# Kernel tuning notes

Hardware: AMD Instinct MI355X
Metric: run time of the kernel (lower is better)

The kernel has to match this reference:

```python
import jax, jax.numpy as jnp
import numpy as np
import math

NUM_HEADS = 8
LN_EPS = 1e-5
SINK_EPS = 1.0  # entropic eps in SinkhornDistance (eps=1)


def _layer_norm(x, g, b):
    m = jnp.mean(x, axis=-1, keepdims=True)
    v = jnp.var(x, axis=-1, keepdims=True)
    return (x - m) * jax.lax.rsqrt(v + LN_EPS) * g + b


def setup_inputs() -> dict:
    key = jax.random.key(0)
    ks = jax.random.split(key, 8)
    B, n, dQ, dV = 8, 1024, 512, 512
    s = 1.0 / math.sqrt(dV)
    return {
        "Q": jax.random.normal(ks[0], (B, n, dQ), jnp.float32),
        "K": jax.random.normal(ks[1], (B, n, dQ), jnp.float32),
        "Wq": jax.random.normal(ks[2], (dV, dQ), jnp.float32) * s,
        "bq": jax.random.normal(ks[3], (dV,), jnp.float32) * 0.01,
        "Wo": jax.random.normal(ks[4], (dV, dV), jnp.float32) * s,
        "bo": jax.random.normal(ks[5], (dV,), jnp.float32) * 0.01,
        "g0": jnp.ones((dV,), jnp.float32),
        "b0": jnp.zeros((dV,), jnp.float32),
        "g1": jnp.ones((dV,), jnp.float32),
        "b1": jnp.zeros((dV,), jnp.float32),
    }


def reference(Q, K, Wq, bq, Wo, bo, g0, b0, g1, b1):
    # K is accepted by the original forward but unused (K_ = V_ = Q_).
    B, n, _ = Q.shape
    dim_V = Wq.shape[0]
    H = NUM_HEADS
    d = dim_V // H

    Qp = Q @ Wq.T + bq                                   # [B, n, dim_V]
    # torch.cat(Q.split(d, 2), 0): head-major stacking -> [H*B, n, d]
    Q_ = Qp.reshape(B, n, H, d).transpose(2, 0, 1, 3).reshape(H * B, n, d)

    sqrtV = math.sqrt(math.sqrt(dim_V))
    X = Q_ / sqrtV
    # cost = dotmat(X, X) = -X X^T  (overall scaled by 1/sqrt(dim_V))
    C = -jnp.einsum('bnd,bmd->bnm', X, X)                # [HB, n, n]

    # log-domain Sinkhorn, eps=1, max_iter=1, mu = nu = 1/n
    log_mu = jnp.log(1.0 / n + 1e-8).astype(Q.dtype)
    M0 = -C / SINK_EPS
    u = SINK_EPS * (log_mu - jax.scipy.special.logsumexp(M0, axis=-1))         # [HB, n]
    v = SINK_EPS * (log_mu - jax.scipy.special.logsumexp(
        (-C + u[:, :, None]) / SINK_EPS, axis=1))                               # [HB, n]
    pi = jnp.exp((-C + u[:, :, None] + v[:, None, :]) / SINK_EPS)               # [HB, n, n]

    A = pi * n
    O_ = Q_ + jnp.einsum('bnm,bmd->bnd', A, Q_)          # [HB, n, d]
    # inverse head stacking -> [B, n, dim_V]
    O = O_.reshape(H, B, n, d).transpose(1, 2, 0, 3).reshape(B, n, dim_V)

    O = _layer_norm(O, g0, b0)
    O = O + jax.nn.relu(O @ Wo.T + bo)
    O = _layer_norm(O, g1, b1)
    return O
```

## Files before the change

kernel.cpp:

```cpp
#include <hip/hip_runtime.h>
#include <hip/hip_bf16.h>

typedef __bf16 bf16;
typedef __bf16 bf16x4 __attribute__((ext_vector_type(4)));
typedef __bf16 bf16x8 __attribute__((ext_vector_type(8)));
typedef float  f32x4  __attribute__((ext_vector_type(4)));
typedef float  f32x16 __attribute__((ext_vector_type(16)));
typedef unsigned int uint32x2 __attribute__((ext_vector_type(2)));

#define DEVI static __device__ __forceinline__

constexpr float SCALE2  = 0.063758716f;
constexpr float L2MU    = -9.9999852f;
constexpr int   LDT     = 72;

DEVI f32x4 mfma16(bf16x8 a, bf16x8 b, f32x4 c) {
    return __builtin_amdgcn_mfma_f32_16x16x32_bf16(a, b, c, 0, 0, 0);
}
DEVI f32x16 mfma32(bf16x8 a, bf16x8 b, f32x16 c) {
    return __builtin_amdgcn_mfma_f32_32x32x16_bf16(a, b, c, 0, 0, 0);
}
DEVI unsigned cvtpk(float lo, float hi) {
    unsigned r;
    asm("v_cvt_pk_bf16_f32 %0, %1, %2" : "=v"(r) : "v"(lo), "v"(hi));
    return r;
}

DEVI bf16x8 cvt8(const float* __restrict__ p) {
    const float4 f0 = *(const float4*)p;
    const float4 f1 = *(const float4*)(p + 4);
    bf16x8 h;
    h[0] = (bf16)f0.x; h[1] = (bf16)f0.y; h[2] = (bf16)f0.z; h[3] = (bf16)f0.w;
    h[4] = (bf16)f1.x; h[5] = (bf16)f1.y; h[6] = (bf16)f1.z; h[7] = (bf16)f1.w;
    return h;
}

__global__ __launch_bounds__(256)
void cvtw_kernel(const float* __restrict__ W, bf16* __restrict__ Wb)
{
    const int i = (blockIdx.x * 256 + threadIdx.x) * 8;
    *(bf16x8*)(&Wb[i]) = cvt8(W + i);
}

template<int EPI>
__global__ __launch_bounds__(256)
void gemm_kernel(const void* __restrict__ Ap, const bf16* __restrict__ Bb,
                 const float* __restrict__ bias, const bf16* __restrict__ X0,
                 bf16* __restrict__ outQh, bf16* __restrict__ outQhT,
                 float* __restrict__ outT)
{
    __shared__ bf16 sA[2][64 * LDT];
    __shared__ bf16 sB[2][64 * LDT];
    const int tid = threadIdx.x;
    const int lin = blockIdx.y * 8 + blockIdx.x;
    const int wk  = ((lin & 7) << 7) | (lin >> 3);
    const int rowBase = (wk >> 3) * 64;
    const int colBase = (wk & 7) * 64;
    const int w = tid >> 6, lane = tid & 63, quad = lane >> 4, l16 = lane & 15;
    const int wr = (w >> 1) * 32, wc = (w & 1) * 32;
    const int r0 = tid >> 3, kb0 = tid & 7;

    f32x4 acc[2][2];
    #pragma unroll
    for (int i = 0; i < 2; ++i)
        #pragma unroll
        for (int j = 0; j < 2; ++j)
            #pragma unroll
            for (int e = 0; e < 4; ++e) acc[i][j][e] = 0.f;

    #pragma unroll
    for (int it = 0; it < 2; ++it) {
        const int r = it * 32 + r0;
        if (EPI == 0)
            *(bf16x8*)(&sA[0][r * LDT + kb0 * 8]) =
                cvt8((const float*)Ap + (size_t)(rowBase + r) * 512 + kb0 * 8);
        else
            *(uint4*)(&sA[0][r * LDT + kb0 * 8]) =
                *(const uint4*)((const bf16*)Ap + (size_t)(rowBase + r) * 512 + kb0 * 8);
        *(uint4*)(&sB[0][r * LDT + kb0 * 8]) =
            *(const uint4*)(Bb + (size_t)(colBase + r) * 512 + kb0 * 8);
    }
    __syncthreads();

    for (int kt8 = 0; kt8 < 8; ++kt8) {
        const int cur = kt8 & 1;
        float4 pfa[2][2];
        uint4  pfa16[2], pfb[2];
        if (kt8 < 7) {
            const int kn = (kt8 + 1) * 64;
            #pragma unroll
            for (int it = 0; it < 2; ++it) {
                const int r = it * 32 + r0;
                if (EPI == 0) {
                    const float* ap = (const float*)Ap + (size_t)(rowBase + r) * 512 + kn + kb0 * 8;
                    pfa[it][0] = *(const float4*)ap;
                    pfa[it][1] = *(const float4*)(ap + 4);
                } else {
                    pfa16[it] = *(const uint4*)((const bf16*)Ap + (size_t)(rowBase + r) * 512 + kn + kb0 * 8);
                }
                pfb[it] = *(const uint4*)(Bb + (size_t)(colBase + r) * 512 + kn + kb0 * 8);
            }
        }

        #pragma unroll
        for (int kk = 0; kk < 2; ++kk) {
            bf16x8 a[2], b[2];
            #pragma unroll
            for (int i = 0; i < 2; ++i)
                a[i] = *(const bf16x8*)(&sA[cur][(wr + i * 16 + l16) * LDT + kk * 32 + quad * 8]);
            #pragma unroll
            for (int j = 0; j < 2; ++j)
                b[j] = *(const bf16x8*)(&sB[cur][(wc + j * 16 + l16) * LDT + kk * 32 + quad * 8]);
            #pragma unroll
            for (int i = 0; i < 2; ++i)
                #pragma unroll
                for (int j = 0; j < 2; ++j)
                    acc[i][j] = mfma16(a[i], b[j], acc[i][j]);
        }

        if (kt8 < 7) {
            #pragma unroll
            for (int it = 0; it < 2; ++it) {
                const int r = it * 32 + r0;
                if (EPI == 0) {
                    bf16x8 h;
                    h[0] = (bf16)pfa[it][0].x; h[1] = (bf16)pfa[it][0].y;
                    h[2] = (bf16)pfa[it][0].z; h[3] = (bf16)pfa[it][0].w;
                    h[4] = (bf16)pfa[it][1].x; h[5] = (bf16)pfa[it][1].y;
                    h[6] = (bf16)pfa[it][1].z; h[7] = (bf16)pfa[it][1].w;
                    *(bf16x8*)(&sA[cur ^ 1][r * LDT + kb0 * 8]) = h;
                } else {
                    *(uint4*)(&sA[cur ^ 1][r * LDT + kb0 * 8]) = pfa16[it];
                }
                *(uint4*)(&sB[cur ^ 1][r * LDT + kb0 * 8]) = pfb[it];
            }
        }
        __syncthreads();
    }

    #pragma unroll
    for (int i = 0; i < 2; ++i) {
        #pragma unroll
        for (int j = 0; j < 2; ++j) {
            const int col = colBase + wc + j * 16 + l16;
            const float bv = bias[col];
            if (EPI == 0) {
                const int hh = col >> 6, jj = col & 63;
                const int rowA = rowBase + wr + i * 16 + quad * 4;
                const int bb = rowA >> 10, iib = rowA & 1023;
                const int bhh = (hh << 3) + bb;
                bf16x4 pk;
                #pragma unroll
                for (int rg = 0; rg < 4; ++rg) {
                    const float z = acc[i][j][rg] + bv;
                    pk[rg] = (bf16)z;
                    outQh[((size_t)(bhh * 1024 + iib + rg) << 6) + jj] = (bf16)z;
                }
                if (outQhT)
                    *(bf16x4*)(&outQhT[(((size_t)bhh * 64 + jj) << 10) + iib]) = pk;
            } else {
                #pragma unroll
                for (int rg = 0; rg < 4; ++rg) {
                    const int row = rowBase + wr + i * 16 + quad * 4 + rg;
                    const float z = acc[i][j][rg] + bv;
                    const float x0 = (float)X0[(size_t)row * 512 + col];
                    outT[(size_t)row * 512 + col] = x0 + fmaxf(z, 0.f);
                }
            }
        }
    }
}

template<int ADD_U>
__global__ __launch_bounds__(256, 4)
void sink_lse_kernel(const bf16* __restrict__ Qh, const float* __restrict__ uin,
                     float* __restrict__ out)
{
    __shared__ bf16 sQm[2][64 * LDT];
    __shared__ float su[1024];
    const int tid = threadIdx.x;
    const int lin = blockIdx.y * 16 + blockIdx.x;
    const int wk  = ((lin & 7) << 7) | (lin >> 3);
    const int bh = wk >> 4;
    const int rowTile = (wk & 15) * 64;
    const bf16* Qb = Qh + ((size_t)bh << 16);

    if (ADD_U)
        *(float4*)(&su[tid * 4]) = *(const float4*)(uin + (bh << 10) + tid * 4);

    const int r0 = tid >> 3, kb0 = tid & 7;
    #pragma unroll
    for (int it = 0; it < 2; ++it)
        *(uint4*)(&sQm[0][(it * 32 + r0) * LDT + kb0 * 8]) =
            *(const uint4*)(Qb + ((it * 32 + r0) << 6) + kb0 * 8);

    const int w = tid >> 6, lane = tid & 63, quad = lane >> 4, l16 = lane & 15;
    bf16x8 afr[2];
    #pragma unroll
    for (int kk = 0; kk < 2; ++kk)
        afr[kk] = *(const bf16x8*)(Qb + ((rowTile + w * 16 + l16) << 6) + kk * 32 + quad * 8);
    __syncthreads();

    float rsum[4] = {0.f, 0.f, 0.f, 0.f};

    for (int mt = 0; mt < 16; ++mt) {
        const int cur = mt & 1;
        uint4 pf[2];
        if (mt < 15) {
            #pragma unroll
            for (int it = 0; it < 2; ++it)
                pf[it] = *(const uint4*)(Qb + (((mt + 1) * 64 + it * 32 + r0) << 6) + kb0 * 8);
        }

        f32x4 acc[4];
        #pragma unroll
        for (int ct = 0; ct < 4; ++ct)
            #pragma unroll
            for (int e = 0; e < 4; ++e) acc[ct][e] = 0.f;

        #pragma unroll
        for (int kk = 0; kk < 2; ++kk) {
            bf16x8 bfr[4];
            #pragma unroll
            for (int ct = 0; ct < 4; ++ct)
                bfr[ct] = *(const bf16x8*)(&sQm[cur][(ct * 16 + l16) * LDT + kk * 32 + quad * 8]);
            #pragma unroll
            for (int ct = 0; ct < 4; ++ct)
                acc[ct] = mfma16(afr[kk], bfr[ct], acc[ct]);
        }
        #pragma unroll
        for (int ct = 0; ct < 4; ++ct) {
            const float uadd = ADD_U ? su[mt * 64 + ct * 16 + l16] : 0.f;
            #pragma unroll
            for (int rg = 0; rg < 4; ++rg)
                rsum[rg] += __builtin_amdgcn_exp2f(fmaf(acc[ct][rg], SCALE2, uadd));
        }

        if (mt < 15) {
            #pragma unroll
            for (int it = 0; it < 2; ++it)
                *(uint4*)(&sQm[cur ^ 1][(it * 32 + r0) * LDT + kb0 * 8]) = pf[it];
        }
        __syncthreads();
    }
    #pragma unroll
    for (int off = 1; off < 16; off <<= 1)
        #pragma unroll
        for (int rg = 0; rg < 4; ++rg)
            rsum[rg] += __shfl_xor(rsum[rg], off);

    if (l16 == 0) {
        #pragma unroll
        for (int rg = 0; rg < 4; ++rg)
            out[(bh << 10) + rowTile + w * 16 + quad * 4 + rg] =
                L2MU - __builtin_amdgcn_logf(rsum[rg]);
    }
}

template<int USE_T>
__global__ __launch_bounds__(256, 2)
void sink_av_kernel(const bf16* __restrict__ Qh, const bf16* __restrict__ QhT,
                    const float* __restrict__ u, const float* __restrict__ v,
                    float* __restrict__ O)
{
    __shared__ bf16 sQi[128 * LDT];
    __shared__ bf16 sQm[2][64 * LDT];
    __shared__ bf16 sQmT[2][64 * LDT];
    __shared__ float sv[1024];
    const int tid = threadIdx.x;
    const int lin = blockIdx.y * 8 + blockIdx.x;
    const int wk  = ((lin & 7) << 6) | (lin >> 3);
    const int bh = wk >> 3;
    const int rowTile = (wk & 7) * 128;
    const bf16* Qb = Qh + ((size_t)bh << 16);
    const bf16* QbT = QhT + ((size_t)bh << 16);
    const int w = tid >> 6, lane = tid & 63, hi = lane >> 5, l31 = lane & 31;
    const int r0 = tid >> 3, kb0 = tid & 7;

    #pragma unroll
    for (int it = 0; it < 4; ++it) {
        int idx = it * 256 + tid;
        int r = idx >> 3, kb = idx & 7;
        *(uint4*)(&sQi[r * LDT + kb * 8]) =
            *(const uint4*)(Qb + ((rowTile + r) << 6) + kb * 8);
    }
    *(float4*)(&sv[tid * 4]) = *(const float4*)(v + (bh << 10) + tid * 4);
    const float u2p = u[(bh << 10) + rowTile + w * 32 + l31] + 10.f;

    #pragma unroll
    for (int it = 0; it < 2; ++it) {
        const int r = it * 32 + r0;
        uint4 val = *(const uint4*)(Qb + (r << 6) + kb0 * 8);
        *(uint4*)(&sQm[0][r * LDT + kb0 * 8]) = val;
        if (USE_T) {
            *(uint4*)(&sQmT[0][r * LDT + kb0 * 8]) =
                *(const uint4*)(QbT + (r << 10) + kb0 * 8);
        } else {
            union { uint4 q; bf16 e[8]; } cv; cv.q = val;
            #pragma unroll
            for (int j = 0; j < 8; ++j)
                sQmT[0][(kb0 * 8 + j) * LDT + r] = cv.e[j];
        }
    }
    __syncthreads();

    f32x16 accO[2];
    #pragma unroll
    for (int dt = 0; dt < 2; ++dt)
        #pragma unroll
        for (int e = 0; e < 16; ++e) accO[dt][e] = 0.f;

    for (int mt = 0; mt < 16; ++mt) {
        const int cur = mt & 1;
        uint4 pfm[2], pft[2];
        if (mt < 15) {
            #pragma unroll
            for (int it = 0; it < 2; ++it) {
                const int r = it * 32 + r0;
                pfm[it] = *(const uint4*)(Qb + (((mt + 1) * 64 + r) << 6) + kb0 * 8);
                if (USE_T)
                    pft[it] = *(const uint4*)(QbT + (r << 10) + (mt + 1) * 64 + kb0 * 8);
            }
        }

        f32x16 accT[2];
        #pragma unroll
        for (int t = 0; t < 2; ++t)
            #pragma unroll
            for (int e = 0; e < 16; ++e) accT[t][e] = 0.f;
        #pragma unroll
        for (int ks = 0; ks < 4; ++ks) {
            const bf16x8 bq = *(const bf16x8*)(&sQi[(w * 32 + l31) * LDT + ks * 16 + hi * 8]);
            #pragma unroll
            for (int t = 0; t < 2; ++t) {
                const bf16x8 am = *(const bf16x8*)(&sQm[cur][(t * 32 + l31) * LDT + ks * 16 + hi * 8]);
                accT[t] = mfma32(am, bq, accT[t]);
            }
        }

        bf16x8 pa[4];
        #pragma unroll
        for (int t = 0; t < 2; ++t) {
            f32x4 vf[4];
            #pragma unroll
            for (int g = 0; g < 4; ++g)
                vf[g] = *(const f32x4*)(&sv[mt * 64 + t * 32 + g * 8 + hi * 4]);
            float p[16];
            #pragma unroll
            for (int r = 0; r < 16; ++r)
                p[r] = __builtin_amdgcn_exp2f(
                         fmaf(accT[t][r], SCALE2, u2p + vf[r >> 2][r & 3]));
            #pragma unroll
            for (int kk = 0; kk < 2; ++kk) {
                const int rb = kk * 8;
                unsigned X0 = cvtpk(p[rb + 0], p[rb + 1]);
                unsigned Y0 = cvtpk(p[rb + 4], p[rb + 5]);
                unsigned X1 = cvtpk(p[rb + 2], p[rb + 3]);
                unsigned Y1 = cvtpk(p[rb + 6], p[rb + 7]);
                uint32x2 s0 = __builtin_amdgcn_permlane32_swap(X0, Y0, false, false);
                uint32x2 s1 = __builtin_amdgcn_permlane32_swap(X1, Y1, false, false);
                union { unsigned wd[4]; bf16x8 v8; } u4;
                u4.wd[0] = s0[0]; u4.wd[1] = s1[0]; u4.wd[2] = s0[1]; u4.wd[3] = s1[1];
                pa[t * 2 + kk] = u4.v8;
            }
        }

        #pragma unroll
        for (int ks = 0; ks < 4; ++ks)
            #pragma unroll
            for (int dt = 0; dt < 2; ++dt) {
                const bf16x8 bt = *(const bf16x8*)(&sQmT[cur][(dt * 32 + l31) * LDT + ks * 16 + hi * 8]);
                accO[dt] = mfma32(pa[ks], bt, accO[dt]);
            }

        if (mt < 15) {
            #pragma unroll
            for (int it = 0; it < 2; ++it) {
                const int r = it * 32 + r0;
                *(uint4*)(&sQm[cur ^ 1][r * LDT + kb0 * 8]) = pfm[it];
                if (USE_T) {
                    *(uint4*)(&sQmT[cur ^ 1][r * LDT + kb0 * 8]) = pft[it];
                } else {
                    union { uint4 q; bf16 e[8]; } cv; cv.q = pfm[it];
                    #pragma unroll
                    for (int j = 0; j < 8; ++j)
                        sQmT[cur ^ 1][(kb0 * 8 + j) * LDT + r] = cv.e[j];
                }
            }
        }
        __syncthreads();
    }

    const int hh = bh >> 3, bb = bh & 7;
    #pragma unroll
    for (int dt = 0; dt < 2; ++dt) {
        const int dcol = dt * 32 + l31;
        #pragma unroll
        for (int r = 0; r < 16; ++r) {
            const int irow = w * 32 + (r & 3) + 8 * (r >> 2) + 4 * hi;
            const float o = (float)sQi[irow * LDT + dcol] + accO[dt][r];
            O[((size_t)(bb * 1024 + rowTile + irow) << 9) + (hh << 6) + dcol] = o;
        }
    }
}

template<typename OutT>
__global__ __launch_bounds__(256)
void ln_kernel(const float* __restrict__ X, const float* __restrict__ g,
               const float* __restrict__ bb, OutT* __restrict__ out)
{
    const int row = blockIdx.x * 4 + (threadIdx.x >> 6);
    const int lane = threadIdx.x & 63;
    const float* x = X + (size_t)row * 512 + lane * 8;
    const float4 a0 = *(const float4*)x;
    const float4 a1 = *(const float4*)(x + 4);
    float s  = a0.x + a0.y + a0.z + a0.w + a1.x + a1.y + a1.z + a1.w;
    float ss = a0.x*a0.x + a0.y*a0.y + a0.z*a0.z + a0.w*a0.w
             + a1.x*a1.x + a1.y*a1.y + a1.z*a1.z + a1.w*a1.w;
    #pragma unroll
    for (int off = 32; off; off >>= 1) {
        s  += __shfl_xor(s, off);
        ss += __shfl_xor(ss, off);
    }
    const float mean = s * (1.f / 512.f);
    const float rstd = rsqrtf(ss * (1.f / 512.f) - mean * mean + 1e-5f);
    const int c = lane * 8;
    const float4 g0 = *(const float4*)(g + c),  g1 = *(const float4*)(g + c + 4);
    const float4 b0 = *(const float4*)(bb + c), b1 = *(const float4*)(bb + c + 4);
    float y[8];
    y[0] = (a0.x - mean) * rstd * g0.x + b0.x;
    y[1] = (a0.y - mean) * rstd * g0.y + b0.y;
    y[2] = (a0.z - mean) * rstd * g0.z + b0.z;
    y[3] = (a0.w - mean) * rstd * g0.w + b0.w;
    y[4] = (a1.x - mean) * rstd * g1.x + b1.x;
    y[5] = (a1.y - mean) * rstd * g1.y + b1.y;
    y[6] = (a1.z - mean) * rstd * g1.z + b1.z;
    y[7] = (a1.w - mean) * rstd * g1.w + b1.w;
    if constexpr (sizeof(OutT) == 2) {
        bf16x8 h;
        #pragma unroll
        for (int j = 0; j < 8; ++j) h[j] = (bf16)y[j];
        *(bf16x8*)((bf16*)out + (size_t)row * 512 + c) = h;
    } else {
        float4 o0 = {y[0], y[1], y[2], y[3]};
        float4 o1 = {y[4], y[5], y[6], y[7]};
        *(float4*)((float*)out + (size_t)row * 512 + c)     = o0;
        *(float4*)((float*)out + (size_t)row * 512 + c + 4) = o1;
    }
}

extern "C" void kernel_launch(void* const* d_in, const int* in_sizes, int n_in,
                              void* d_out, int out_size, void* d_ws, size_t ws_size,
                              hipStream_t stream)
{
    const float* Q  = (const float*)d_in[0];
    const float* Wq = (const float*)d_in[2];
    const float* bq = (const float*)d_in[3];
    const float* Wo = (const float*)d_in[4];
    const float* bo = (const float*)d_in[5];
    const float* g0 = (const float*)d_in[6];
    const float* b0 = (const float*)d_in[7];
    const float* g1 = (const float*)d_in[8];
    const float* b1 = (const float*)d_in[9];

    char* ws = (char*)d_ws;
    const bool useT = ws_size >= (size_t)34078720;

    bf16 *Qh, *QhT, *X0, *Wqb, *Wob;
    float *u, *v, *Obuf;
    if (useT) {
        Qh   = (bf16*)ws;
        QhT  = (bf16*)(ws + 8388608);
        X0   = (bf16*)(ws + 8388608);
        u    = (float*)(ws + 16777216);
        v    = (float*)(ws + 17039360);
        Obuf = (float*)(ws + 17301504);
        Wqb  = (bf16*)(ws + 16777216);
        Wob  = (bf16*)ws;
    } else {
        Qh   = (bf16*)ws;
        QhT  = nullptr;
        X0   = (bf16*)ws;
        u    = (float*)(ws + 8388608);
        v    = (float*)(ws + 8650752);
        Obuf = (float*)(ws + 8912896);
        Wqb  = (bf16*)(ws + 8388608);
        Wob  = (bf16*)(ws + 8388608);
    }

    cvtw_kernel<<<128, 256, 0, stream>>>(Wq, Wqb);
    gemm_kernel<0><<<dim3(8, 128), 256, 0, stream>>>(Q, Wqb, bq, nullptr, Qh, QhT, nullptr);
    sink_lse_kernel<0><<<dim3(16, 64), 256, 0, stream>>>(Qh, nullptr, u);
    sink_lse_kernel<1><<<dim3(16, 64), 256, 0, stream>>>(Qh, u, v);
    if (useT)
        sink_av_kernel<1><<<dim3(8, 64), 256, 0, stream>>>(Qh, QhT, u, v, Obuf);
    else
        sink_av_kernel<0><<<dim3(8, 64), 256, 0, stream>>>(Qh, Qh, u, v, Obuf);
    cvtw_kernel<<<128, 256, 0, stream>>>(Wo, Wob);
    ln_kernel<bf16><<<2048, 256, 0, stream>>>(Obuf, g0, b0, X0);
    gemm_kernel<1><<<dim3(8, 128), 256, 0, stream>>>(X0, Wob, bo, X0, nullptr, nullptr, Obuf);
    ln_kernel<float><<<2048, 256, 0, stream>>>(Obuf, g1, b1, (float*)d_out);
}
```

Measured before the change: 199.6 us.

## Restructure Sinkhorn LSE kernel to direct-global 32x32 MFMA without LDS staging

The LSE kernel no longer stages key tiles in double-buffered shared memory with per-tile barriers. Each wave now holds a 32-row query fragment in registers and reads key fragments straight from global memory (L1/L2 cached). It uses 32x32 MFMA and splits the key tiles between wave pairs, with one shared-memory reduction at the end. The AV kernel also hoists the query-fragment LDS loads out of the inner loop into registers. This removes barrier and LDS traffic, but it relies on cache hits for repeated global loads and raises register use.

```diff
diff --git a/kernel.cpp b/kernel.cpp
--- a/kernel.cpp
+++ b/kernel.cpp
@@ -176,8 +176,8 @@
 void sink_lse_kernel(const bf16* __restrict__ Qh, const float* __restrict__ uin,
                      float* __restrict__ out)
 {
-    __shared__ bf16 sQm[2][64 * LDT];
     __shared__ float su[1024];
+    __shared__ float sred[4][64];
     const int tid = threadIdx.x;
     const int lin = blockIdx.y * 16 + blockIdx.x;
     const int wk  = ((lin & 7) << 7) | (lin >> 3);
@@ -185,75 +185,54 @@
     const int rowTile = (wk & 15) * 64;
     const bf16* Qb = Qh + ((size_t)bh << 16);
 
-    if (ADD_U)
+    const int w = tid >> 6, lane = tid & 63, hi = lane >> 5, l31 = lane & 31;
+    const int rg = w & 1, mh = w >> 1;
+
+    if (ADD_U) {
         *(float4*)(&su[tid * 4]) = *(const float4*)(uin + (bh << 10) + tid * 4);
-
-    const int r0 = tid >> 3, kb0 = tid & 7;
-    #pragma unroll
-    for (int it = 0; it < 2; ++it)
-        *(uint4*)(&sQm[0][(it * 32 + r0) * LDT + kb0 * 8]) =
-            *(const uint4*)(Qb + ((it * 32 + r0) << 6) + kb0 * 8);
-
-    const int w = tid >> 6, lane = tid & 63, quad = lane >> 4, l16 = lane & 15;
-    bf16x8 afr[2];
-    #pragma unroll
-    for (int kk = 0; kk < 2; ++kk)
-        afr[kk] = *(const bf16x8*)(Qb + ((rowTile + w * 16 + l16) << 6) + kk * 32 + quad * 8);
+        __syncthreads();
+    }
+
+    bf16x8 bq[4];
+    #pragma unroll
+    for (int ks = 0; ks < 4; ++ks)
+        bq[ks] = *(const bf16x8*)(Qb + ((rowTile + rg * 32 + l31) << 6) + ks * 16 + hi * 8);
+
+    float rsum = 0.f;
+    for (int mt = mh; mt < 16; mt += 2) {
+        #pragma unroll
+        for (int t = 0; t < 2; ++t) {
+            f32x16 accT;
+            #pragma unroll
+            for (int e = 0; e < 16; ++e) accT[e] = 0.f;
+            #pragma unroll
+            for (int ks = 0; ks < 4; ++ks) {
+                const bf16x8 am = *(const bf16x8*)(
+                    Qb + ((mt * 64 + t * 32 + l31) << 6) + ks * 16 + hi * 8);
+                accT = mfma32(am, bq[ks], accT);
+            }
+            if (ADD_U) {
+                f32x4 vf[4];
+                #pragma unroll
+                for (int g = 0; g < 4; ++g)
+                    vf[g] = *(const f32x4*)(&su[mt * 64 + t * 32 + g * 8 + hi * 4]);
+                #pragma unroll
+                for (int r = 0; r < 16; ++r)
+                    rsum += __builtin_amdgcn_exp2f(
+                        fmaf(accT[r], SCALE2, vf[r >> 2][r & 3]));
+            } else {
+                #pragma unroll
+                for (int r = 0; r < 16; ++r)
+                    rsum += __builtin_amdgcn_exp2f(accT[r] * SCALE2);
+            }
+        }
+    }
+    sred[w][lane] = rsum;
     __syncthreads();
-
-    float rsum[4] = {0.f, 0.f, 0.f, 0.f};
-
-    for (int mt = 0; mt < 16; ++mt) {
-        const int cur = mt & 1;
-        uint4 pf[2];
-        if (mt < 15) {
-            #pragma unroll
-            for (int it = 0; it < 2; ++it)
-                pf[it] = *(const uint4*)(Qb + (((mt + 1) * 64 + it * 32 + r0) << 6) + kb0 * 8);
-        }
-
-        f32x4 acc[4];
-        #pragma unroll
-        for (int ct = 0; ct < 4; ++ct)
-            #pragma unroll
-            for (int e = 0; e < 4; ++e) acc[ct][e] = 0.f;
-
-        #pragma unroll
-        for (int kk = 0; kk < 2; ++kk) {
-            bf16x8 bfr[4];
-            #pragma unroll
-            for (int ct = 0; ct < 4; ++ct)
-                bfr[ct] = *(const bf16x8*)(&sQm[cur][(ct * 16 + l16) * LDT + kk * 32 + quad * 8]);
-            #pragma unroll
-            for (int ct = 0; ct < 4; ++ct)
-                acc[ct] = mfma16(afr[kk], bfr[ct], acc[ct]);
-        }
-        #pragma unroll
-        for (int ct = 0; ct < 4; ++ct) {
-            const float uadd = ADD_U ? su[mt * 64 + ct * 16 + l16] : 0.f;
-            #pragma unroll
-            for (int rg = 0; rg < 4; ++rg)
-                rsum[rg] += __builtin_amdgcn_exp2f(fmaf(acc[ct][rg], SCALE2, uadd));
-        }
-
-        if (mt < 15) {
-            #pragma unroll
-            for (int it = 0; it < 2; ++it)
-                *(uint4*)(&sQm[cur ^ 1][(it * 32 + r0) * LDT + kb0 * 8]) = pf[it];
-        }
-        __syncthreads();
-    }
-    #pragma unroll
-    for (int off = 1; off < 16; off <<= 1)
-        #pragma unroll
-        for (int rg = 0; rg < 4; ++rg)
-            rsum[rg] += __shfl_xor(rsum[rg], off);
-
-    if (l16 == 0) {
-        #pragma unroll
-        for (int rg = 0; rg < 4; ++rg)
-            out[(bh << 10) + rowTile + w * 16 + quad * 4 + rg] =
-                L2MU - __builtin_amdgcn_logf(rsum[rg]);
+    if (w < 2 && lane < 32) {
+        const float t = sred[w][l31] + sred[w][l31 + 32]
+                      + sred[w + 2][l31] + sred[w + 2][l31 + 32];
+        out[(bh << 10) + rowTile + w * 32 + l31] = L2MU - __builtin_amdgcn_logf(t);
     }
 }
 
@@ -304,6 +283,11 @@
     }
     __syncthreads();
 
+    bf16x8 bq[4];
+    #pragma unroll
+    for (int ks = 0; ks < 4; ++ks)
+        bq[ks] = *(const bf16x8*)(&sQi[(w * 32 + l31) * LDT + ks * 16 + hi * 8]);
+
     f32x16 accO[2];
     #pragma unroll
     for (int dt = 0; dt < 2; ++dt)
@@ -330,11 +314,10 @@
             for (int e = 0; e < 16; ++e) accT[t][e] = 0.f;
         #pragma unroll
         for (int ks = 0; ks < 4; ++ks) {
-            const bf16x8 bq = *(const bf16x8*)(&sQi[(w * 32 + l31) * LDT + ks * 16 + hi * 8]);
             #pragma unroll
             for (int t = 0; t < 2; ++t) {
                 const bf16x8 am = *(const bf16x8*)(&sQm[cur][(t * 32 + l31) * LDT + ks * 16 + hi * 8]);
-                accT[t] = mfma32(am, bq, accT[t]);
+                accT[t] = mfma32(am, bq[ks], accT[t]);
             }
         }
 
```

New measurement: 226.8 us. +13.6%, slower.
